# Performance work log

Hardware: AMD Instinct MI355X
Metric: run time of the kernel (lower is better)

Reference implementation:

```python
import jax, jax.numpy as jnp
import numpy as np

B, T, I = 8, 8192, 128
E, J, K = 16, 128, 1024


def setup_inputs() -> dict:
    key = jax.random.key(0)
    k1, k2, k3 = jax.random.split(key, 3)
    X = jax.random.normal(k1, (B, T, I), dtype=jnp.float32)
    ind = jax.random.randint(k2, (B, E, K), 0, T, dtype=jnp.int64)
    # matches torch.rand(E, I, J): uniform [0, 1)
    W = jax.random.uniform(k3, (E, I, J), dtype=jnp.float32)
    return {"X": X, "ind": ind, "W": W}


def reference(X, ind, W):
    # Dense per-expert matmul over ALL tokens: Y[b,e,t,j] = sum_i X[b,t,i] W[e,i,j]
    # (torch expand is a broadcast view; einsum broadcasts directly)
    Y = jnp.einsum('bti,eij->betj', X, W)  # [B, E, T, J]
    # Gather selected tokens per (batch, expert) along the token axis
    Yg = jnp.take_along_axis(Y, ind[..., None], axis=2)  # [B, E, K, J]
    return Yg
```

## Files before the change

### kernel.cpp

```cpp
#include <hip/hip_runtime.h>

#define B_ 8
#define T_ 8192
#define I_ 128
#define E_ 16
#define J_ 128
#define K_ 1024
#define ROWS 128

typedef unsigned short u16;
typedef unsigned int   u32;
typedef __attribute__((ext_vector_type(8))) short s8v;
typedef __attribute__((ext_vector_type(4))) float f4v;

__device__ __forceinline__ u16 f2bf(float f) {
    union { float f; u32 u; } v; v.f = f;
    const u32 u = v.u;
    return (u16)((u + 0x7fffu + ((u >> 16) & 1u)) >> 16);
}

__global__ void convert_wt(const float* __restrict__ W, u16* __restrict__ Wt) {
    const int t  = blockIdx.x * 256 + threadIdx.x;
    const int o8 = t * 8;
    const int e  = o8 >> 14;
    const int r  = o8 & 16383;
    const int j  = r >> 7;
    const int i0 = r & 127;
    const float* Wp = W + e * (I_ * J_) + j;
    s8v o;
#pragma unroll
    for (int u = 0; u < 8; ++u)
        o[u] = (short)f2bf(Wp[(i0 + u) * J_]);
    *reinterpret_cast<s8v*>(Wt + o8) = o;
}

template<bool PRE>
__global__ __launch_bounds__(512, 4)
void gather_mfma(const float* __restrict__ X, const int* __restrict__ ind,
                 const void* __restrict__ Wsrc, float* __restrict__ Y) {
    __shared__ u16 WsT[I_ * J_];
    __shared__ u16 Xs[ROWS * I_];

    const int t    = threadIdx.x;
    const int wave = t >> 6;
    const int lane = t & 63;

    const int orig = blockIdx.x;
    const int bid  = (orig & 7) * 128 + (orig >> 3);
    const int kt = bid & 7;
    const int be = bid >> 3;
    const int e  = be & (E_ - 1);
    const int b  = be >> 4;
    const int k0 = kt * ROWS;

    if (PRE) {
        const s8v* Wg = reinterpret_cast<const s8v*>((const u16*)Wsrc + (size_t)e * (I_ * J_));
#pragma unroll
        for (int u = 0; u < 4; ++u) {
            const int c   = t + 512 * u;
            const int row = c >> 4;
            const s8v v = Wg[c];
            *reinterpret_cast<s8v*>((char*)WsT + ((c * 16) ^ ((row & 7) << 4))) = v;
        }
    } else {
        const float* We = (const float*)Wsrc + (size_t)e * (I_ * J_);
#pragma unroll
        for (int u = 0; u < 8; ++u) {
            const int f4i = t + 512 * u;
            const int i   = f4i >> 5;
            const int j0  = (f4i & 31) * 4;
            const float4 w4 = reinterpret_cast<const float4*>(We)[f4i];
            const float ws[4] = {w4.x, w4.y, w4.z, w4.w};
#pragma unroll
            for (int q = 0; q < 4; ++q) {
                const int j = j0 + q;
                *(u16*)((char*)WsT + ((j * 256 + i * 2) ^ ((j & 7) << 4))) = f2bf(ws[q]);
            }
        }
    }

    {
        const int r   = t >> 2;
        const int q   = t & 3;
        const int idx = ind[(size_t)be * K_ + k0 + r];
        const float4* Xr = reinterpret_cast<const float4*>(X + ((size_t)b * T_ + idx) * I_) + q * 8;
        const int sx = (r & 7) << 4;
        char* xrow = (char*)Xs + r * 256;
#pragma unroll
        for (int u = 0; u < 4; ++u) {
            const float4 a = Xr[2 * u], c = Xr[2 * u + 1];
            s8v o;
            o[0] = (short)f2bf(a.x); o[1] = (short)f2bf(a.y);
            o[2] = (short)f2bf(a.z); o[3] = (short)f2bf(a.w);
            o[4] = (short)f2bf(c.x); o[5] = (short)f2bf(c.y);
            o[6] = (short)f2bf(c.z); o[7] = (short)f2bf(c.w);
            *reinterpret_cast<s8v*>(xrow + ((q * 64 + u * 16) ^ sx)) = o;
        }
    }
    __syncthreads();

    const int rq  = wave >> 1;
    const int jh  = wave & 1;
    const int g   = lane >> 4;
    const int l15 = lane & 15;
    const int sx  = (lane & 7) << 4;

    f4v acc[2][4];
#pragma unroll
    for (int tr = 0; tr < 2; ++tr)
#pragma unroll
        for (int n = 0; n < 4; ++n)
#pragma unroll
            for (int r = 0; r < 4; ++r) acc[tr][n][r] = 0.f;

    const char* xb = (const char*)Xs  + (size_t)(rq * 32 + l15) * 256;
    const char* wb = (const char*)WsT + (size_t)(jh * 64 + l15) * 256;
#pragma unroll
    for (int s = 0; s < 4; ++s) {
        const int off = (s * 64 + g * 16) ^ sx;
        const s8v a0 = *reinterpret_cast<const s8v*>(xb + off);
        const s8v a1 = *reinterpret_cast<const s8v*>(xb + 16 * 256 + off);
#pragma unroll
        for (int n = 0; n < 4; ++n) {
            const s8v bf = *reinterpret_cast<const s8v*>(wb + n * 16 * 256 + off);
            acc[0][n] = __builtin_amdgcn_mfma_f32_16x16x32_bf16(a0, bf, acc[0][n], 0, 0, 0);
            acc[1][n] = __builtin_amdgcn_mfma_f32_16x16x32_bf16(a1, bf, acc[1][n], 0, 0, 0);
        }
    }

    float* Yb = Y + ((size_t)be * K_ + k0) * J_;
#pragma unroll
    for (int tr = 0; tr < 2; ++tr)
#pragma unroll
        for (int n = 0; n < 4; ++n) {
            const int col = jh * 64 + n * 16 + l15;
            const int row0 = rq * 32 + tr * 16 + g * 4;
#pragma unroll
            for (int r = 0; r < 4; ++r)
                Yb[(size_t)(row0 + r) * J_ + col] = acc[tr][n][r];
        }
}

extern "C" void kernel_launch(void* const* d_in, const int* in_sizes, int n_in,
                              void* d_out, int out_size, void* d_ws, size_t ws_size,
                              hipStream_t stream) {
    (void)in_sizes; (void)n_in; (void)out_size;
    const float* X   = (const float*)d_in[0];
    const int*   ind = (const int*)d_in[1];
    const float* W   = (const float*)d_in[2];
    float*       Y   = (float*)d_out;

    const size_t wt_bytes = (size_t)E_ * I_ * J_ * sizeof(u16);
    const int grid = B_ * E_ * (K_ / ROWS);

    if (ws_size >= wt_bytes && d_ws != nullptr) {
        u16* Wt = (u16*)d_ws;
        hipLaunchKernelGGL(convert_wt, dim3(E_ * I_ * J_ / (256 * 8)), dim3(256), 0, stream, W, Wt);
        hipLaunchKernelGGL((gather_mfma<true>), dim3(grid), dim3(512), 0, stream,
                           X, ind, (const void*)Wt, Y);
    } else {
        hipLaunchKernelGGL((gather_mfma<false>), dim3(grid), dim3(512), 0, stream,
                           X, ind, (const void*)W, Y);
    }
}
```

Before: 29.86 us.

## Keep expert weight fragments in registers and stream gathered rows without LDS

Adds a kernel that loads each wave's bf16 weight fragments straight from global memory into registers once. It then loops over 16-row strips of gathered X, converting them to bf16 in registers and issuing MFMAs, with no shared memory or block barrier. The grid shrinks to 512 blocks of 256 threads, each covering 256 rows, which removes LDS staging and synchronisation. In exchange it uses more registers, has fewer blocks in flight to hide the scattered X loads, and each wave's X loads are serialized per strip.

```diff
diff --git a/kernel.cpp b/kernel.cpp
--- a/kernel.cpp
+++ b/kernel.cpp
@@ -6,7 +6,6 @@
 #define E_ 16
 #define J_ 128
 #define K_ 1024
-#define ROWS 128
 
 typedef unsigned short u16;
 typedef unsigned int   u32;
@@ -34,12 +33,90 @@
     *reinterpret_cast<s8v*>(Wt + o8) = o;
 }
 
-template<bool PRE>
+__global__ __launch_bounds__(256, 3)
+void gather_mfma_regw(const float* __restrict__ X, const int* __restrict__ ind,
+                      const u16* __restrict__ Wt, float* __restrict__ Y) {
+    const int t    = threadIdx.x;
+    const int wave = t >> 6;
+    const int lane = t & 63;
+
+    const int orig = blockIdx.x;
+    const int bid  = (orig & 7) * 64 + (orig >> 3);
+    const int kq = bid & 3;
+    const int be = bid >> 2;
+    const int e  = be & (E_ - 1);
+    const int b  = be >> 4;
+
+    const int rh  = wave >> 1;
+    const int jh  = wave & 1;
+    const int g   = lane >> 4;
+    const int l15 = lane & 15;
+
+    const u16* Wte = Wt + (size_t)e * (I_ * J_);
+    s8v wf[4][4];
+#pragma unroll
+    for (int nj = 0; nj < 4; ++nj)
+#pragma unroll
+        for (int s = 0; s < 4; ++s)
+            wf[nj][s] = *reinterpret_cast<const s8v*>(
+                Wte + (size_t)(jh * 64 + nj * 16 + l15) * I_ + s * 32 + g * 8);
+
+    const int rbase = kq * 256 + rh * 128;
+    int idx8[8];
+#pragma unroll
+    for (int st = 0; st < 8; ++st)
+        idx8[st] = ind[(size_t)be * K_ + rbase + st * 16 + l15];
+
+    const float* Xb = X + (size_t)b * T_ * I_;
+    float* Ybase = Y + ((size_t)be * K_ + rbase) * J_ + jh * 64;
+
+#pragma unroll
+    for (int st = 0; st < 8; ++st) {
+        const float4* xr = reinterpret_cast<const float4*>(Xb + (size_t)idx8[st] * I_);
+        float4 xv[8];
+#pragma unroll
+        for (int s = 0; s < 4; ++s) {
+            xv[2 * s]     = xr[s * 8 + g * 2];
+            xv[2 * s + 1] = xr[s * 8 + g * 2 + 1];
+        }
+        s8v xf[4];
+#pragma unroll
+        for (int s = 0; s < 4; ++s) {
+            const float4 a = xv[2 * s], c = xv[2 * s + 1];
+            xf[s][0] = (short)f2bf(a.x); xf[s][1] = (short)f2bf(a.y);
+            xf[s][2] = (short)f2bf(a.z); xf[s][3] = (short)f2bf(a.w);
+            xf[s][4] = (short)f2bf(c.x); xf[s][5] = (short)f2bf(c.y);
+            xf[s][6] = (short)f2bf(c.z); xf[s][7] = (short)f2bf(c.w);
+        }
+
+        f4v acc[4];
+#pragma unroll
+        for (int nj = 0; nj < 4; ++nj)
+#pragma unroll
+            for (int rr = 0; rr < 4; ++rr) acc[nj][rr] = 0.f;
+
+#pragma unroll
+        for (int s = 0; s < 4; ++s)
+#pragma unroll
+            for (int nj = 0; nj < 4; ++nj)
+                acc[nj] = __builtin_amdgcn_mfma_f32_16x16x32_bf16(xf[s], wf[nj][s], acc[nj], 0, 0, 0);
+
+        float* Yst = Ybase + (size_t)(st * 16 + g * 4) * J_;
+#pragma unroll
+        for (int nj = 0; nj < 4; ++nj) {
+            const int col = nj * 16 + l15;
+#pragma unroll
+            for (int rr = 0; rr < 4; ++rr)
+                Yst[(size_t)rr * J_ + col] = acc[nj][rr];
+        }
+    }
+}
+
 __global__ __launch_bounds__(512, 4)
-void gather_mfma(const float* __restrict__ X, const int* __restrict__ ind,
-                 const void* __restrict__ Wsrc, float* __restrict__ Y) {
+void gather_mfma_lds(const float* __restrict__ X, const int* __restrict__ ind,
+                     const float* __restrict__ Wsrc, float* __restrict__ Y) {
     __shared__ u16 WsT[I_ * J_];
-    __shared__ u16 Xs[ROWS * I_];
+    __shared__ u16 Xs[128 * I_];
 
     const int t    = threadIdx.x;
     const int wave = t >> 6;
@@ -51,19 +128,10 @@
     const int be = bid >> 3;
     const int e  = be & (E_ - 1);
     const int b  = be >> 4;
-    const int k0 = kt * ROWS;
-
-    if (PRE) {
-        const s8v* Wg = reinterpret_cast<const s8v*>((const u16*)Wsrc + (size_t)e * (I_ * J_));
-#pragma unroll
-        for (int u = 0; u < 4; ++u) {
-            const int c   = t + 512 * u;
-            const int row = c >> 4;
-            const s8v v = Wg[c];
-            *reinterpret_cast<s8v*>((char*)WsT + ((c * 16) ^ ((row & 7) << 4))) = v;
-        }
-    } else {
-        const float* We = (const float*)Wsrc + (size_t)e * (I_ * J_);
+    const int k0 = kt * 128;
+
+    {
+        const float* We = Wsrc + (size_t)e * (I_ * J_);
 #pragma unroll
         for (int u = 0; u < 8; ++u) {
             const int f4i = t + 512 * u;
@@ -78,7 +146,6 @@
             }
         }
     }
-
     {
         const int r   = t >> 2;
         const int q   = t & 3;
@@ -151,15 +218,14 @@
     float*       Y   = (float*)d_out;
 
     const size_t wt_bytes = (size_t)E_ * I_ * J_ * sizeof(u16);
-    const int grid = B_ * E_ * (K_ / ROWS);
 
     if (ws_size >= wt_bytes && d_ws != nullptr) {
         u16* Wt = (u16*)d_ws;
         hipLaunchKernelGGL(convert_wt, dim3(E_ * I_ * J_ / (256 * 8)), dim3(256), 0, stream, W, Wt);
-        hipLaunchKernelGGL((gather_mfma<true>), dim3(grid), dim3(512), 0, stream,
-                           X, ind, (const void*)Wt, Y);
+        hipLaunchKernelGGL(gather_mfma_regw, dim3(B_ * E_ * 4), dim3(256), 0, stream,
+                           X, ind, Wt, Y);
     } else {
-        hipLaunchKernelGGL((gather_mfma<false>), dim3(grid), dim3(512), 0, stream,
-                           X, ind, (const void*)W, Y);
-    }
-}
+        hipLaunchKernelGGL(gather_mfma_lds, dim3(B_ * E_ * (K_ / 128)), dim3(512), 0, stream,
+                           X, ind, W, Y);
+    }
+}
```

New measurement: 35.02 us. 1.17x slower.

## Load gathered X rows straight into registers with double-buffered stripes, skipping LDS

Applied to the files above, without the earlier changes.

The main path becomes a new kernel with 256 threads that stages only the bf16 weight tile in LDS. Each wave loads its gathered X rows from global memory directly into registers as MFMA A-operands, in 16-row stripes with two buffers so the next stripe's load overlaps the current stripe's compute and store. This removes the X LDS staging, its barrier and the LDS footprint, but each lane now fetches scattered row fragments itself and holds more registers. The fallback path keeps the old LDS kernel.

```diff
diff --git a/kernel.cpp b/kernel.cpp
--- a/kernel.cpp
+++ b/kernel.cpp
@@ -6,7 +6,6 @@
 #define E_ 16
 #define J_ 128
 #define K_ 1024
-#define ROWS 128
 
 typedef unsigned short u16;
 typedef unsigned int   u32;
@@ -34,12 +33,48 @@
     *reinterpret_cast<s8v*>(Wt + o8) = o;
 }
 
-template<bool PRE>
-__global__ __launch_bounds__(512, 4)
-void gather_mfma(const float* __restrict__ X, const int* __restrict__ ind,
-                 const void* __restrict__ Wsrc, float* __restrict__ Y) {
+#define LOAD_STRIPE(buf, st) {                                                  \
+    const float4* xr_ = reinterpret_cast<const float4*>(Xb + (size_t)idx[st] * I_); \
+    _Pragma("unroll")                                                           \
+    for (int u_ = 0; u_ < 8; ++u_)                                              \
+        buf[u_] = xr_[(u_ >> 1) * 8 + g * 2 + (u_ & 1)];                        \
+}
+
+#define COMPUTE_STORE(buf, st) {                                                \
+    f4v acc_[4];                                                                \
+    _Pragma("unroll")                                                           \
+    for (int n_ = 0; n_ < 4; ++n_)                                              \
+        _Pragma("unroll")                                                       \
+        for (int r_ = 0; r_ < 4; ++r_) acc_[n_][r_] = 0.f;                      \
+    _Pragma("unroll")                                                           \
+    for (int s_ = 0; s_ < 4; ++s_) {                                            \
+        const float4 a_ = buf[2 * s_], c_ = buf[2 * s_ + 1];                    \
+        s8v xf_;                                                                \
+        xf_[0] = (short)f2bf(a_.x); xf_[1] = (short)f2bf(a_.y);                 \
+        xf_[2] = (short)f2bf(a_.z); xf_[3] = (short)f2bf(a_.w);                 \
+        xf_[4] = (short)f2bf(c_.x); xf_[5] = (short)f2bf(c_.y);                 \
+        xf_[6] = (short)f2bf(c_.z); xf_[7] = (short)f2bf(c_.w);                 \
+        const int off_ = (s_ * 64 + g * 16) ^ sx;                               \
+        _Pragma("unroll")                                                       \
+        for (int n_ = 0; n_ < 4; ++n_) {                                        \
+            const s8v bf_ = *reinterpret_cast<const s8v*>(wb + n_ * 16 * 256 + off_); \
+            acc_[n_] = __builtin_amdgcn_mfma_f32_16x16x32_bf16(xf_, bf_, acc_[n_], 0, 0, 0); \
+        }                                                                       \
+    }                                                                           \
+    float* Yst_ = Ybase + (size_t)((st) * 16 + g * 4) * J_;                     \
+    _Pragma("unroll")                                                           \
+    for (int n_ = 0; n_ < 4; ++n_) {                                            \
+        const int col_ = n_ * 16 + l15;                                         \
+        _Pragma("unroll")                                                       \
+        for (int r_ = 0; r_ < 4; ++r_)                                          \
+            Yst_[(size_t)r_ * J_ + col_] = acc_[n_][r_];                        \
+    }                                                                           \
+}
+
+__global__ __launch_bounds__(256, 4)
+void gather_mfma_direct(const float* __restrict__ X, const int* __restrict__ ind,
+                        const u16* __restrict__ Wt, float* __restrict__ Y) {
     __shared__ u16 WsT[I_ * J_];
-    __shared__ u16 Xs[ROWS * I_];
 
     const int t    = threadIdx.x;
     const int wave = t >> 6;
@@ -51,19 +86,66 @@
     const int be = bid >> 3;
     const int e  = be & (E_ - 1);
     const int b  = be >> 4;
-    const int k0 = kt * ROWS;
-
-    if (PRE) {
-        const s8v* Wg = reinterpret_cast<const s8v*>((const u16*)Wsrc + (size_t)e * (I_ * J_));
-#pragma unroll
-        for (int u = 0; u < 4; ++u) {
-            const int c   = t + 512 * u;
+    const int k0 = kt * 128;
+
+    {
+        const s8v* Wg = reinterpret_cast<const s8v*>(Wt + (size_t)e * (I_ * J_));
+#pragma unroll
+        for (int u = 0; u < 8; ++u) {
+            const int c   = t + 256 * u;
             const int row = c >> 4;
             const s8v v = Wg[c];
             *reinterpret_cast<s8v*>((char*)WsT + ((c * 16) ^ ((row & 7) << 4))) = v;
         }
-    } else {
-        const float* We = (const float*)Wsrc + (size_t)e * (I_ * J_);
+    }
+    __syncthreads();
+
+    const int rh  = wave >> 1;
+    const int jh  = wave & 1;
+    const int g   = lane >> 4;
+    const int l15 = lane & 15;
+    const int sx  = (lane & 7) << 4;
+    const char* wb = (const char*)WsT + (size_t)(jh * 64 + l15) * 256;
+
+    const float* Xb = X + (size_t)b * T_ * I_;
+    float* Ybase = Y + ((size_t)be * K_ + k0 + rh * 64) * J_ + jh * 64;
+
+    const size_t indbase = (size_t)be * K_ + k0 + rh * 64 + l15;
+    int idx[4];
+#pragma unroll
+    for (int st = 0; st < 4; ++st) idx[st] = ind[indbase + st * 16];
+
+    float4 bufA[8], bufB[8];
+    LOAD_STRIPE(bufA, 0);
+    LOAD_STRIPE(bufB, 1);
+    COMPUTE_STORE(bufA, 0);
+    LOAD_STRIPE(bufA, 2);
+    COMPUTE_STORE(bufB, 1);
+    LOAD_STRIPE(bufB, 3);
+    COMPUTE_STORE(bufA, 2);
+    COMPUTE_STORE(bufB, 3);
+}
+
+__global__ __launch_bounds__(512, 4)
+void gather_mfma_lds(const float* __restrict__ X, const int* __restrict__ ind,
+                     const float* __restrict__ Wsrc, float* __restrict__ Y) {
+    __shared__ u16 WsT[I_ * J_];
+    __shared__ u16 Xs[128 * I_];
+
+    const int t    = threadIdx.x;
+    const int wave = t >> 6;
+    const int lane = t & 63;
+
+    const int orig = blockIdx.x;
+    const int bid  = (orig & 7) * 128 + (orig >> 3);
+    const int kt = bid & 7;
+    const int be = bid >> 3;
+    const int e  = be & (E_ - 1);
+    const int b  = be >> 4;
+    const int k0 = kt * 128;
+
+    {
+        const float* We = Wsrc + (size_t)e * (I_ * J_);
 #pragma unroll
         for (int u = 0; u < 8; ++u) {
             const int f4i = t + 512 * u;
@@ -78,7 +160,6 @@
             }
         }
     }
-
     {
         const int r   = t >> 2;
         const int q   = t & 3;
@@ -151,15 +232,14 @@
     float*       Y   = (float*)d_out;
 
     const size_t wt_bytes = (size_t)E_ * I_ * J_ * sizeof(u16);
-    const int grid = B_ * E_ * (K_ / ROWS);
 
     if (ws_size >= wt_bytes && d_ws != nullptr) {
         u16* Wt = (u16*)d_ws;
         hipLaunchKernelGGL(convert_wt, dim3(E_ * I_ * J_ / (256 * 8)), dim3(256), 0, stream, W, Wt);
-        hipLaunchKernelGGL((gather_mfma<true>), dim3(grid), dim3(512), 0, stream,
-                           X, ind, (const void*)Wt, Y);
+        hipLaunchKernelGGL(gather_mfma_direct, dim3(1024), dim3(256), 0, stream,
+                           X, ind, Wt, Y);
     } else {
-        hipLaunchKernelGGL((gather_mfma<false>), dim3(grid), dim3(512), 0, stream,
-                           X, ind, (const void*)W, Y);
-    }
-}
+        hipLaunchKernelGGL(gather_mfma_lds, dim3(1024), dim3(512), 0, stream,
+                           X, ind, W, Y);
+    }
+}
```

Result: slower. 33.57 us (+12.4%).

## Pre-swizzle weight image and load it into LDS via direct global-to-LDS loads

Applied to the files above, without the earlier changes.

The weight conversion kernel now transposes through shared memory with coalesced float4 reads, and writes a bf16 image already in the XOR-swizzled LDS layout. The main kernel then copies that image straight into LDS with global_load_lds 16-byte loads, skipping the register round trip and the per-thread swizzle math. The index load is also hoisted before the weight copy so its latency overlaps it. The risk is that the convert kernel's much smaller grid (64 blocks) may take longer per launch.

```diff
diff --git a/kernel.cpp b/kernel.cpp
--- a/kernel.cpp
+++ b/kernel.cpp
@@ -19,19 +19,43 @@
     return (u16)((u + 0x7fffu + ((u >> 16) & 1u)) >> 16);
 }
 
+__device__ __forceinline__ void gload_lds16(const void* g, void* l) {
+    __builtin_amdgcn_global_load_lds(
+        (const __attribute__((address_space(1))) u32*)g,
+        (__attribute__((address_space(3))) u32*)l, 16, 0, 0);
+}
+
 __global__ void convert_wt(const float* __restrict__ W, u16* __restrict__ Wt) {
-    const int t  = blockIdx.x * 256 + threadIdx.x;
-    const int o8 = t * 8;
-    const int e  = o8 >> 14;
-    const int r  = o8 & 16383;
-    const int j  = r >> 7;
-    const int i0 = r & 127;
-    const float* Wp = W + e * (I_ * J_) + j;
-    s8v o;
+    __shared__ float Wf[I_ * 33];
+    const int bid = blockIdx.x;
+    const int e   = bid >> 2;
+    const int j0  = (bid & 3) * 32;
+    const int t   = threadIdx.x;
+    const float* We = W + (size_t)e * (I_ * J_);
 #pragma unroll
-    for (int u = 0; u < 8; ++u)
-        o[u] = (short)f2bf(Wp[(i0 + u) * J_]);
-    *reinterpret_cast<s8v*>(Wt + o8) = o;
+    for (int u = 0; u < 4; ++u) {
+        const int f4 = t + 256 * u;
+        const int i  = f4 >> 3;
+        const int c  = f4 & 7;
+        const float4 v = *reinterpret_cast<const float4*>(We + (size_t)i * J_ + j0 + c * 4);
+        float* p = &Wf[i * 33 + c * 4];
+        p[0] = v.x; p[1] = v.y; p[2] = v.z; p[3] = v.w;
+    }
+    __syncthreads();
+    char* img = (char*)Wt + (size_t)e * (I_ * J_ * 2);
+#pragma unroll
+    for (int u2 = 0; u2 < 2; ++u2) {
+        const int c  = t + 256 * u2;
+        const int jl = c >> 4;
+        const int j  = j0 + jl;
+        const int i0 = (c & 15) * 8;
+        s8v o;
+#pragma unroll
+        for (int u = 0; u < 8; ++u)
+            o[u] = (short)f2bf(Wf[(i0 + u) * 33 + jl]);
+        const int cimg = j * 16 + (c & 15);
+        *reinterpret_cast<s8v*>(img + ((cimg * 16) ^ ((j & 7) << 4))) = o;
+    }
 }
 
 template<bool PRE>
@@ -53,14 +77,16 @@
     const int b  = be >> 4;
     const int k0 = kt * ROWS;
 
+    const int r   = t >> 2;
+    const int q   = t & 3;
+    const int idx = ind[(size_t)be * K_ + k0 + r];
+
     if (PRE) {
-        const s8v* Wg = reinterpret_cast<const s8v*>((const u16*)Wsrc + (size_t)e * (I_ * J_));
+        const char* Wimg = (const char*)Wsrc + (size_t)e * 32768;
 #pragma unroll
         for (int u = 0; u < 4; ++u) {
-            const int c   = t + 512 * u;
-            const int row = c >> 4;
-            const s8v v = Wg[c];
-            *reinterpret_cast<s8v*>((char*)WsT + ((c * 16) ^ ((row & 7) << 4))) = v;
+            const int off = (wave * 4 + u) * 1024;
+            gload_lds16(Wimg + off + lane * 16, (char*)WsT + off);
         }
     } else {
         const float* We = (const float*)Wsrc + (size_t)e * (I_ * J_);
@@ -72,17 +98,14 @@
             const float4 w4 = reinterpret_cast<const float4*>(We)[f4i];
             const float ws[4] = {w4.x, w4.y, w4.z, w4.w};
 #pragma unroll
-            for (int q = 0; q < 4; ++q) {
-                const int j = j0 + q;
-                *(u16*)((char*)WsT + ((j * 256 + i * 2) ^ ((j & 7) << 4))) = f2bf(ws[q]);
+            for (int qq = 0; qq < 4; ++qq) {
+                const int j = j0 + qq;
+                *(u16*)((char*)WsT + ((j * 256 + i * 2) ^ ((j & 7) << 4))) = f2bf(ws[qq]);
             }
         }
     }
 
     {
-        const int r   = t >> 2;
-        const int q   = t & 3;
-        const int idx = ind[(size_t)be * K_ + k0 + r];
         const float4* Xr = reinterpret_cast<const float4*>(X + ((size_t)b * T_ + idx) * I_) + q * 8;
         const int sx = (r & 7) << 4;
         char* xrow = (char*)Xs + r * 256;
@@ -111,7 +134,7 @@
 #pragma unroll
         for (int n = 0; n < 4; ++n)
 #pragma unroll
-            for (int r = 0; r < 4; ++r) acc[tr][n][r] = 0.f;
+            for (int rr = 0; rr < 4; ++rr) acc[tr][n][rr] = 0.f;
 
     const char* xb = (const char*)Xs  + (size_t)(rq * 32 + l15) * 256;
     const char* wb = (const char*)WsT + (size_t)(jh * 64 + l15) * 256;
@@ -136,8 +159,8 @@
             const int col = jh * 64 + n * 16 + l15;
             const int row0 = rq * 32 + tr * 16 + g * 4;
 #pragma unroll
-            for (int r = 0; r < 4; ++r)
-                Yb[(size_t)(row0 + r) * J_ + col] = acc[tr][n][r];
+            for (int rr = 0; rr < 4; ++rr)
+                Yb[(size_t)(row0 + rr) * J_ + col] = acc[tr][n][rr];
         }
 }
 
@@ -155,7 +178,7 @@
 
     if (ws_size >= wt_bytes && d_ws != nullptr) {
         u16* Wt = (u16*)d_ws;
-        hipLaunchKernelGGL(convert_wt, dim3(E_ * I_ * J_ / (256 * 8)), dim3(256), 0, stream, W, Wt);
+        hipLaunchKernelGGL(convert_wt, dim3(E_ * 4), dim3(256), 0, stream, W, Wt);
         hipLaunchKernelGGL((gather_mfma<true>), dim3(grid), dim3(512), 0, stream,
                            X, ind, (const void*)Wt, Y);
     } else {
```

After: 30.74 us. 1.03x slower.
